# Kernel optimization log

Measured on AMD Instinct MI355X. Metric: run time of the kernel, lower is better.

The kernel has to match this reference:

```python
import jax, jax.numpy as jnp
import numpy as np

B, L, D = 8, 128, 768  # batch, max_len, in_features == out_features


def setup_inputs() -> dict:
    key = jax.random.key(0)
    k1, k2, k3, k4, k5 = jax.random.split(key, 5)
    text = jax.random.normal(k1, (B, L, D), dtype=jnp.float32)
    adj = jax.random.uniform(k2, (B, L, L), dtype=jnp.float32)
    dep_embed = jax.random.normal(k3, (B, L, L, D), dtype=jnp.float32)
    # kaiming_uniform-ish init scale for weight, small bias
    bound_w = 1.0 / np.sqrt(D)
    weight = jax.random.uniform(k4, (D, D), minval=-bound_w, maxval=bound_w, dtype=jnp.float32)
    bias = jax.random.uniform(k5, (D,), minval=-bound_w, maxval=bound_w, dtype=jnp.float32)
    return {"text": text, "adj": adj, "dep_embed": dep_embed, "weight": weight, "bias": bias}


def reference(text, adj, dep_embed, weight, bias):
    # Original math: out[b,i,:] = relu(sum_j adj[b,i,j] * ((text[b,j]+dep_embed[b,j,i]) @ W) + bias)
    # Fused form: aggregate first (linear in j), then apply the single GEMM with W.
    agg = jnp.einsum('bij,bjd->bid', adj, text)              # neighbor-sum of node feats
    agg = agg + jnp.einsum('bij,bjid->bid', adj, dep_embed)  # neighbor-sum of edge-type embeds
    out = jnp.einsum('bid,de->bie', agg, weight) + bias
    return jax.nn.relu(out)
```

## Files before the change

kernel.cpp:

```cpp
#include <hip/hip_runtime.h>

#define B_ 8
#define L_ 128
#define D_ 768

typedef float v4f __attribute__((ext_vector_type(4)));

__global__ __launch_bounds__(192) void agg_kernel(
    const float* __restrict__ text,
    const float* __restrict__ adj,
    const float* __restrict__ dep,
    float* __restrict__ agg) {
  const int bi = blockIdx.x;
  const int b  = bi >> 7;
  const int i  = bi & (L_ - 1);
  const int t  = threadIdx.x;

  __shared__ float adj_s[L_];
  if (t < L_) adj_s[t] = adj[(size_t)bi * L_ + t];
  __syncthreads();

  const v4f* text4 = (const v4f*)(text + (size_t)b * L_ * D_);
  const v4f* dep4  = (const v4f*)(dep + ((size_t)(b * L_) * L_ + i) * D_);

  v4f acc = {0.f, 0.f, 0.f, 0.f};
#pragma unroll 8
  for (int j = 0; j < L_; ++j) {
    const float a  = adj_s[j];
    const v4f   tx = text4[j * (D_ / 4) + t];
    const v4f   dv = __builtin_nontemporal_load(&dep4[(size_t)j * (L_ * D_ / 4) + t]);
    acc += a * (tx + dv);
  }
  ((v4f*)(agg + (size_t)bi * D_))[t] = acc;
}

#define TM 32
#define TN 64
#define TK 32
#define NKT (D_ / TK)

__global__ __launch_bounds__(256) void gemm_bias_relu(
    const float* __restrict__ A,
    const float* __restrict__ W,
    const float* __restrict__ bias,
    float* __restrict__ out) {
  __shared__ float AsT[TK][TM + 2];
  __shared__ float Bs[TK][TN];

  const int tid = threadIdx.x;
  const int tx  = tid & 15;
  const int ty  = tid >> 4;
  const int m0  = blockIdx.y * TM;
  const int n0  = blockIdx.x * TN;

  const int ar  = tid >> 3;
  const int ac  = (tid & 7) * 4;
  const int br  = tid >> 4;
  const int bc  = (tid & 15) * 4;

  const float* Arow = A + (size_t)(m0 + ar) * D_ + ac;
  const float* Wrow0 = W + (size_t)br * D_ + n0 + bc;
  const float* Wrow1 = W + (size_t)(br + 16) * D_ + n0 + bc;

  float acc[2][4] = {};

  v4f a_reg  = *(const v4f*)Arow;
  v4f b_reg0 = *(const v4f*)Wrow0;
  v4f b_reg1 = *(const v4f*)Wrow1;

  for (int t = 0; t < NKT; ++t) {
    __syncthreads();
    AsT[ac + 0][ar] = a_reg.x;
    AsT[ac + 1][ar] = a_reg.y;
    AsT[ac + 2][ar] = a_reg.z;
    AsT[ac + 3][ar] = a_reg.w;
    *(v4f*)&Bs[br][bc]      = b_reg0;
    *(v4f*)&Bs[br + 16][bc] = b_reg1;
    __syncthreads();

    if (t + 1 < NKT) {
      a_reg  = *(const v4f*)(Arow + (t + 1) * TK);
      b_reg0 = *(const v4f*)(Wrow0 + (size_t)(t + 1) * TK * D_);
      b_reg1 = *(const v4f*)(Wrow1 + (size_t)(t + 1) * TK * D_);
    }

#pragma unroll
    for (int kk = 0; kk < TK; ++kk) {
      const float2 av = *(const float2*)&AsT[kk][ty * 2];
      const v4f    bv = *(const v4f*)&Bs[kk][tx * 4];
#pragma unroll
      for (int pn = 0; pn < 4; ++pn) {
        acc[0][pn] += av.x * bv[pn];
        acc[1][pn] += av.y * bv[pn];
      }
    }
  }

  const v4f bvec = *(const v4f*)&bias[n0 + tx * 4];
#pragma unroll
  for (int pm = 0; pm < 2; ++pm) {
    v4f o;
#pragma unroll
    for (int pn = 0; pn < 4; ++pn) o[pn] = fmaxf(acc[pm][pn] + bvec[pn], 0.f);
    *(v4f*)&out[(size_t)(m0 + ty * 2 + pm) * D_ + n0 + tx * 4] = o;
  }
}

extern "C" void kernel_launch(void* const* d_in, const int* in_sizes, int n_in,
                              void* d_out, int out_size, void* d_ws, size_t ws_size,
                              hipStream_t stream) {
  const float* text   = (const float*)d_in[0];
  const float* adj    = (const float*)d_in[1];
  const float* dep    = (const float*)d_in[2];
  const float* weight = (const float*)d_in[3];
  const float* bias   = (const float*)d_in[4];
  float* out = (float*)d_out;
  float* agg = (float*)d_ws;

  agg_kernel<<<B_ * L_, 192, 0, stream>>>(text, adj, dep, agg);

  dim3 grid(D_ / TN, (B_ * L_) / TM);
  gemm_bias_relu<<<grid, 256, 0, stream>>>(agg, weight, bias, out);
}
```

Measured before the change: 547.4 us.

## Split agg over j halves with paired rows and explicit prefetch, sum partials in GEMM

The aggregation kernel now has each block handle two adjacent rows i and one half of the j range. It reads two contiguous dep_embed rows per j and software-prefetches them in groups of four. The two j-half partial sums go to separate workspace buffers, and the GEMM adds them while loading its A tiles. The aim is more contiguous, better-overlapped streaming of the large dep_embed tensor, paid for with a doubled workspace, an extra A read stream in the GEMM, and more registers.

```diff
diff --git a/kernel.cpp b/kernel.cpp
--- a/kernel.cpp
+++ b/kernel.cpp
@@ -3,6 +3,8 @@
 #define B_ 8
 #define L_ 128
 #define D_ 768
+#define JH 64
+#define UN 4
 
 typedef float v4f __attribute__((ext_vector_type(4)));
 
@@ -10,28 +12,66 @@
     const float* __restrict__ text,
     const float* __restrict__ adj,
     const float* __restrict__ dep,
-    float* __restrict__ agg) {
-  const int bi = blockIdx.x;
-  const int b  = bi >> 7;
-  const int i  = bi & (L_ - 1);
+    float* __restrict__ P) {
+  const int bx = blockIdx.x;
+  const int jh = bx & 1;
+  const int p  = (bx >> 1) & 63;
+  const int b  = bx >> 7;
+  const int i0 = p * 2;
   const int t  = threadIdx.x;
+  const int j0 = jh * JH;
 
-  __shared__ float adj_s[L_];
-  if (t < L_) adj_s[t] = adj[(size_t)bi * L_ + t];
+  __shared__ float a_s[JH][2];
+  if (t < 2 * JH) {
+    const int r  = t >> 6;
+    const int jj = t & 63;
+    a_s[jj][r] = adj[((size_t)b * L_ + i0 + r) * L_ + j0 + jj];
+  }
   __syncthreads();
 
-  const v4f* text4 = (const v4f*)(text + (size_t)b * L_ * D_);
-  const v4f* dep4  = (const v4f*)(dep + ((size_t)(b * L_) * L_ + i) * D_);
+  const v4f* dep4 = (const v4f*)(dep + (((size_t)b * L_ + j0) * L_ + i0) * D_);
+  const size_t jstr = (size_t)L_ * D_ / 4;
 
-  v4f acc = {0.f, 0.f, 0.f, 0.f};
+  v4f acc0 = {0.f, 0.f, 0.f, 0.f};
+  v4f acc1 = {0.f, 0.f, 0.f, 0.f};
+
+  v4f c0[UN], c1[UN];
+#pragma unroll
+  for (int u = 0; u < UN; ++u) {
+    c0[u] = __builtin_nontemporal_load(&dep4[(size_t)u * jstr + t]);
+    c1[u] = __builtin_nontemporal_load(&dep4[(size_t)u * jstr + (D_ / 4) + t]);
+  }
+  for (int jb = 0; jb < JH; jb += UN) {
+    v4f n0[UN], n1[UN];
+    if (jb + UN < JH) {
+#pragma unroll
+      for (int u = 0; u < UN; ++u) {
+        n0[u] = __builtin_nontemporal_load(&dep4[(size_t)(jb + UN + u) * jstr + t]);
+        n1[u] = __builtin_nontemporal_load(&dep4[(size_t)(jb + UN + u) * jstr + (D_ / 4) + t]);
+      }
+    }
+#pragma unroll
+    for (int u = 0; u < UN; ++u) {
+      const float2 av = *(const float2*)&a_s[jb + u][0];
+      acc0 += av.x * c0[u];
+      acc1 += av.y * c1[u];
+    }
+#pragma unroll
+    for (int u = 0; u < UN; ++u) { c0[u] = n0[u]; c1[u] = n1[u]; }
+  }
+
+  const v4f* text4 = (const v4f*)(text + ((size_t)b * L_ + j0) * D_);
 #pragma unroll 8
-  for (int j = 0; j < L_; ++j) {
-    const float a  = adj_s[j];
-    const v4f   tx = text4[j * (D_ / 4) + t];
-    const v4f   dv = __builtin_nontemporal_load(&dep4[(size_t)j * (L_ * D_ / 4) + t]);
-    acc += a * (tx + dv);
+  for (int j = 0; j < JH; ++j) {
+    const float2 av = *(const float2*)&a_s[j][0];
+    const v4f tx = text4[(size_t)j * (D_ / 4) + t];
+    acc0 += av.x * tx;
+    acc1 += av.y * tx;
   }
-  ((v4f*)(agg + (size_t)bi * D_))[t] = acc;
+
+  float* Prow = P + ((size_t)jh * (B_ * L_) + (size_t)b * L_ + i0) * D_;
+  ((v4f*)Prow)[t] = acc0;
+  ((v4f*)Prow)[D_ / 4 + t] = acc1;
 }
 
 #define TM 32
@@ -40,7 +80,7 @@
 #define NKT (D_ / TK)
 
 __global__ __launch_bounds__(256) void gemm_bias_relu(
-    const float* __restrict__ A,
+    const float* __restrict__ P,
     const float* __restrict__ W,
     const float* __restrict__ bias,
     float* __restrict__ out) {
@@ -58,28 +98,32 @@
   const int br  = tid >> 4;
   const int bc  = (tid & 15) * 4;
 
-  const float* Arow = A + (size_t)(m0 + ar) * D_ + ac;
+  const float* A0row = P + (size_t)(m0 + ar) * D_ + ac;
+  const float* A1row = A0row + (size_t)(B_ * L_) * D_;
   const float* Wrow0 = W + (size_t)br * D_ + n0 + bc;
   const float* Wrow1 = W + (size_t)(br + 16) * D_ + n0 + bc;
 
   float acc[2][4] = {};
 
-  v4f a_reg  = *(const v4f*)Arow;
+  v4f a0_reg = *(const v4f*)A0row;
+  v4f a1_reg = *(const v4f*)A1row;
   v4f b_reg0 = *(const v4f*)Wrow0;
   v4f b_reg1 = *(const v4f*)Wrow1;
 
   for (int t = 0; t < NKT; ++t) {
     __syncthreads();
-    AsT[ac + 0][ar] = a_reg.x;
-    AsT[ac + 1][ar] = a_reg.y;
-    AsT[ac + 2][ar] = a_reg.z;
-    AsT[ac + 3][ar] = a_reg.w;
+    const v4f asum = a0_reg + a1_reg;
+    AsT[ac + 0][ar] = asum.x;
+    AsT[ac + 1][ar] = asum.y;
+    AsT[ac + 2][ar] = asum.z;
+    AsT[ac + 3][ar] = asum.w;
     *(v4f*)&Bs[br][bc]      = b_reg0;
     *(v4f*)&Bs[br + 16][bc] = b_reg1;
     __syncthreads();
 
     if (t + 1 < NKT) {
-      a_reg  = *(const v4f*)(Arow + (t + 1) * TK);
+      a0_reg = *(const v4f*)(A0row + (t + 1) * TK);
+      a1_reg = *(const v4f*)(A1row + (t + 1) * TK);
       b_reg0 = *(const v4f*)(Wrow0 + (size_t)(t + 1) * TK * D_);
       b_reg1 = *(const v4f*)(Wrow1 + (size_t)(t + 1) * TK * D_);
     }
@@ -115,10 +159,10 @@
   const float* weight = (const float*)d_in[3];
   const float* bias   = (const float*)d_in[4];
   float* out = (float*)d_out;
-  float* agg = (float*)d_ws;
+  float* P   = (float*)d_ws;
 
-  agg_kernel<<<B_ * L_, 192, 0, stream>>>(text, adj, dep, agg);
+  agg_kernel<<<B_ * L_ * 2 / 2, 192, 0, stream>>>(text, adj, dep, P);
 
   dim3 grid(D_ / TN, (B_ * L_) / TM);
-  gemm_bias_relu<<<grid, 256, 0, stream>>>(agg, weight, bias, out);
+  gemm_bias_relu<<<grid, 256, 0, stream>>>(P, weight, bias, out);
 }
```

New measurement: 542.2 us. Within noise of the previous version (-0.9%).

## Split aggregation over j-chunks with partial sums and a separate reduction kernel

Applied to the files above, without the earlier changes.

The aggregation kernel now gives each block a tile of 16 target rows i and a chunk of 8 source nodes j, reusing each text row across 16 i values and reading 16 contiguous dep rows per j. Each chunk writes partial sums to a workspace buffer, and a new reduce kernel adds the 16 partials into the aggregate before the GEMM. The goal is more contiguous, coalesced streaming of the large dep_embed tensor and fewer redundant text loads. In exchange it adds about 50 MB of partial-sum traffic, an extra kernel launch, and a larger workspace requirement, and it drops the nontemporal load hint.

```diff
diff --git a/kernel.cpp b/kernel.cpp
--- a/kernel.cpp
+++ b/kernel.cpp
@@ -3,35 +3,79 @@
 #define B_ 8
 #define L_ 128
 #define D_ 768
+#define D4 (D_ / 4)
+#define IT 16
+#define JC 8
+#define NS (L_ / JC)
 
 typedef float v4f __attribute__((ext_vector_type(4)));
 
-__global__ __launch_bounds__(192) void agg_kernel(
+__global__ __launch_bounds__(256) void agg_kernel(
     const float* __restrict__ text,
     const float* __restrict__ adj,
     const float* __restrict__ dep,
-    float* __restrict__ agg) {
-  const int bi = blockIdx.x;
-  const int b  = bi >> 7;
-  const int i  = bi & (L_ - 1);
+    float* __restrict__ P) {
+  const int bx = blockIdx.x;
+  const int it = bx & 7;
+  const int s  = (bx >> 3) & 15;
+  const int b  = bx >> 7;
+  const int i0 = it * IT;
+  const int j0 = s * JC;
   const int t  = threadIdx.x;
+  const int iq = t >> 6;
+  const int dq = t & 63;
 
-  __shared__ float adj_s[L_];
-  if (t < L_) adj_s[t] = adj[(size_t)bi * L_ + t];
+  __shared__ float adj_s[JC][IT];
+  if (t < JC * IT) {
+    const int j = t >> 4;
+    const int i = t & 15;
+    adj_s[j][i] = adj[((size_t)b * L_ + i0 + i) * L_ + j0 + j];
+  }
   __syncthreads();
 
-  const v4f* text4 = (const v4f*)(text + (size_t)b * L_ * D_);
-  const v4f* dep4  = (const v4f*)(dep + ((size_t)(b * L_) * L_ + i) * D_);
+  const v4f* dep4  = (const v4f*)dep + ((size_t)b * L_ + j0) * L_ * D4;
+  const v4f* text4 = (const v4f*)text + ((size_t)b * L_ + j0) * D4;
 
-  v4f acc = {0.f, 0.f, 0.f, 0.f};
-#pragma unroll 8
-  for (int j = 0; j < L_; ++j) {
-    const float a  = adj_s[j];
-    const v4f   tx = text4[j * (D_ / 4) + t];
-    const v4f   dv = __builtin_nontemporal_load(&dep4[(size_t)j * (L_ * D_ / 4) + t]);
-    acc += a * (tx + dv);
+  v4f acc[4][3] = {};
+
+#pragma unroll
+  for (int j = 0; j < JC; ++j) {
+    float a[4];
+#pragma unroll
+    for (int k = 0; k < 4; ++k) a[k] = adj_s[j][iq + 4 * k];
+
+    v4f tx[3];
+#pragma unroll
+    for (int c = 0; c < 3; ++c) tx[c] = text4[(size_t)j * D4 + dq + 64 * c];
+
+#pragma unroll
+    for (int k = 0; k < 4; ++k) {
+      const v4f* drow = dep4 + ((size_t)j * L_ + i0 + iq + 4 * k) * D4;
+#pragma unroll
+      for (int c = 0; c < 3; ++c) {
+        const v4f dv = drow[dq + 64 * c];
+        acc[k][c] += a[k] * (tx[c] + dv);
+      }
+    }
   }
-  ((v4f*)(agg + (size_t)bi * D_))[t] = acc;
+
+  float* Pb = P + ((size_t)s * (B_ * L_) + (size_t)b * L_ + i0) * D_;
+#pragma unroll
+  for (int k = 0; k < 4; ++k)
+#pragma unroll
+    for (int c = 0; c < 3; ++c)
+      ((v4f*)Pb)[(size_t)(iq + 4 * k) * D4 + dq + 64 * c] = acc[k][c];
+}
+
+__global__ __launch_bounds__(256) void reduce_kernel(
+    const float* __restrict__ P,
+    float* __restrict__ agg) {
+  const size_t idx = (size_t)blockIdx.x * 256 + threadIdx.x;
+  const v4f* P4 = (const v4f*)P;
+  v4f sum = P4[idx];
+#pragma unroll
+  for (int k = 1; k < NS; ++k) sum += P4[(size_t)k * ((size_t)B_ * L_ * D4) + idx];
+  ((v4f*)agg)[idx] = sum;
 }
 
 #define TM 32
@@ -58,7 +102,7 @@
   const int br  = tid >> 4;
   const int bc  = (tid & 15) * 4;
 
-  const float* Arow = A + (size_t)(m0 + ar) * D_ + ac;
+  const float* Arow  = A + (size_t)(m0 + ar) * D_ + ac;
   const float* Wrow0 = W + (size_t)br * D_ + n0 + bc;
   const float* Wrow1 = W + (size_t)(br + 16) * D_ + n0 + bc;
 
@@ -115,10 +159,13 @@
   const float* weight = (const float*)d_in[3];
   const float* bias   = (const float*)d_in[4];
   float* out = (float*)d_out;
-  float* agg = (float*)d_ws;
 
-  agg_kernel<<<B_ * L_, 192, 0, stream>>>(text, adj, dep, agg);
+  float* P    = (float*)d_ws;
+  float* aggb = P + (size_t)NS * B_ * L_ * D_;
+
+  agg_kernel<<<B_ * L_ * NS / IT, 256, 0, stream>>>(text, adj, dep, P);
+  reduce_kernel<<<(B_ * L_ * D4) / 256, 256, 0, stream>>>(P, aggb);
 
   dim3 grid(D_ / TN, (B_ * L_) / TM);
-  gemm_bias_relu<<<grid, 256, 0, stream>>>(agg, weight, bias, out);
+  gemm_bias_relu<<<grid, 256, 0, stream>>>(aggb, weight, bias, out);
 }
```

Measured after the change: 582.3 us. +6.4%, slower.
